# Optimization experiments

Hardware: AMD Instinct MI355X
Metric: run time of the kernel (lower is better)

## Reference

```python
import jax, jax.numpy as jnp
import numpy as np

NUM_USERS = 100000
NUM_PROTO = 16
EMBD_DIM = 128
BATCH = 8192
SEQ = 50
MOMENTUM = 0.9


def _l2norm(x, axis=-1, eps=1e-12):
    # matches torch F.normalize: x / max(||x||, eps)
    n = jnp.linalg.norm(x, axis=axis, keepdims=True)
    return x / jnp.maximum(n, eps)


def setup_inputs() -> dict:
    key = jax.random.key(0)
    k1, k2, k3, k4, k5 = jax.random.split(key, 5)
    user_idx = jnp.arange(BATCH, dtype=jnp.int64 if jax.config.jax_enable_x64 else jnp.int32)
    features = jax.random.normal(k1, (BATCH, SEQ, EMBD_DIM), dtype=jnp.float32)
    success_mask = jax.random.uniform(k2, (BATCH, SEQ), dtype=jnp.float32)
    user_prototypes = jax.random.normal(k3, (NUM_USERS, NUM_PROTO, EMBD_DIM), dtype=jnp.float32)
    shared_prototypes = jax.random.normal(k4, (1, NUM_PROTO, EMBD_DIM), dtype=jnp.float32)
    interaction_count = jax.random.uniform(k5, (NUM_USERS,), dtype=jnp.float32) * 500.0
    return {
        "user_idx": user_idx,
        "features": features,
        "success_mask": success_mask,
        "user_prototypes": user_prototypes,
        "shared_prototypes": shared_prototypes,
        "interaction_count": interaction_count,
    }


def reference(user_idx, features, success_mask, user_prototypes, shared_prototypes, interaction_count):
    # ---- get_prototypes: gather + curriculum blend ----
    cnt = interaction_count[user_idx]                          # [B]
    w = jax.nn.sigmoid(cnt / 100.0 - 3.0)[:, None, None]       # [B,1,1]
    user_p = user_prototypes[user_idx]                         # [B,P,D] gather
    combined = w * user_p + (1.0 - w) * shared_prototypes      # [B,P,D]

    # ---- update_prototypes: momentum blend + normalize + scatter ----
    m = jnp.clip(MOMENTUM + cnt / 1000.0, MOMENTUM, 0.99)[:, None, None]  # [B,1,1]
    sm = success_mask[..., None]                               # [B,S,1]
    masked = features * sm                                     # [B,S,D]
    denom = jnp.maximum(jnp.sum(sm, axis=1), 1e-6)             # [B,1]
    upd = jnp.sum(masked, axis=1) / denom                      # [B,D]
    upd = _l2norm(upd)                                         # [B,D]
    upd_b = jnp.broadcast_to(upd[:, None, :], (upd.shape[0], NUM_PROTO, upd.shape[1]))  # [B,P,D]

    new_rows = m * user_p + (1.0 - m) * upd_b                  # [B,P,D]
    new_user_prototypes = user_prototypes.at[user_idx].set(new_rows)  # scatter write-back

    shared_upd = _l2norm(jnp.mean(upd_b, axis=0))              # [P,D]
    new_shared = MOMENTUM * shared_prototypes + (1.0 - MOMENTUM) * shared_upd[None]  # [1,P,D]

    new_interaction_count = interaction_count.at[user_idx].add(1.0)
    return combined, new_rows, new_user_prototypes, new_shared, new_interaction_count
```

## Files before the change

kernel.cpp:

```cpp
#include <hip/hip_runtime.h>

#define BATCH   8192
#define SEQ     50
#define DIM     128
#define NPROTO  16
#define NUSERS  100000
#define ROWF4   (NPROTO * DIM / 4)
#define DF4     (DIM / 4)

typedef float vf4 __attribute__((ext_vector_type(4)));

__global__ void k_fill_inv(int* __restrict__ inv) {
    int i = blockIdx.x * blockDim.x + threadIdx.x;
    if (i < NUSERS) inv[i] = -1;
}

__global__ void k_prep(const int* __restrict__ idx, const float* __restrict__ icount,
                       int* __restrict__ inv, float2* __restrict__ wm) {
    int b = blockIdx.x * blockDim.x + threadIdx.x;
    if (b >= BATCH) return;
    int u = idx[b];
    inv[u] = b;
    float cnt = icount[u];
    float w = 1.0f / (1.0f + expf(3.0f - cnt * 0.01f));
    float m = fminf(fmaxf(0.9f + cnt * 0.001f, 0.9f), 0.99f);
    wm[b] = make_float2(w, m);
}

__global__ void k_upd(const float* __restrict__ feat, const float* __restrict__ mask,
                      float* __restrict__ upd) {
    int t = threadIdx.x;
    int bb = t >> 5;
    int l = t & 31;
    int b = blockIdx.x * 4 + bb;
    const vf4* f4p = (const vf4*)(feat + (size_t)b * SEQ * DIM);
    const float* mk = mask + (size_t)b * SEQ;
    vf4 acc = {0.f, 0.f, 0.f, 0.f};
    float msum = 0.f;
    #pragma unroll 5
    for (int s = 0; s < SEQ; ++s) {
        float m = mk[s];
        vf4 v = __builtin_nontemporal_load(&f4p[s * DF4 + l]);
        acc += v * m;
        msum += m;
    }
    float inv_d = 1.0f / fmaxf(msum, 1e-6f);
    acc *= inv_d;
    float sq = acc.x*acc.x + acc.y*acc.y + acc.z*acc.z + acc.w*acc.w;
    for (int off = 16; off >= 1; off >>= 1)
        sq += __shfl_xor(sq, off, 32);
    float inv = 1.0f / fmaxf(sqrtf(sq), 1e-12f);
    acc *= inv;
    ((vf4*)(upd + (size_t)b * DIM))[l] = acc;
}

__global__ void k_partial(const float* __restrict__ upd, float* __restrict__ part) {
    int d = threadIdx.x;
    int j = blockIdx.x;
    float acc = 0.f;
    for (int b = j; b < BATCH; b += 128)
        acc += upd[(size_t)b * DIM + d];
    part[j * DIM + d] = acc;
}

__global__ void k_shared(const float* __restrict__ part, const float* __restrict__ sharedP,
                         float* __restrict__ out4) {
    __shared__ float red[DIM];
    int d = threadIdx.x;
    float s = 0.f;
    for (int j = 0; j < 128; ++j) s += part[j * DIM + d];
    float mean = s * (1.0f / (float)BATCH);
    red[d] = mean * mean;
    __syncthreads();
    for (int off = 64; off >= 1; off >>= 1) {
        if (d < off) red[d] += red[d + off];
        __syncthreads();
    }
    float normed = mean / fmaxf(sqrtf(red[0]), 1e-12f);
    for (int p = 0; p < NPROTO; ++p)
        out4[p * DIM + d] = 0.9f * sharedP[p * DIM + d] + 0.1f * normed;
}

__global__ void __launch_bounds__(256) k_mega(
        const int* __restrict__ inv, const float2* __restrict__ wm,
        const vf4* __restrict__ userP, const vf4* __restrict__ sharedP,
        const vf4* __restrict__ upd,
        vf4* __restrict__ out1, vf4* __restrict__ out2, vf4* __restrict__ out3) {
    int u = blockIdx.x;
    int b = inv[u];
    size_t base = (size_t)u * ROWF4;
    if (b < 0) {
        #pragma unroll
        for (int k = 0; k < 2; ++k) {
            int i = threadIdx.x + k * 256;
            vf4 v = __builtin_nontemporal_load(&userP[base + i]);
            __builtin_nontemporal_store(v, &out3[base + i]);
        }
    } else {
        float2 c2 = wm[b];
        float w = c2.x, m = c2.y;
        float w1 = 1.0f - w, m1 = 1.0f - m;
        size_t ob = (size_t)b * ROWF4;
        const vf4* ub = upd + (size_t)b * DF4;
        #pragma unroll
        for (int k = 0; k < 2; ++k) {
            int i = threadIdx.x + k * 256;
            vf4 p  = __builtin_nontemporal_load(&userP[base + i]);
            vf4 sh = sharedP[i];
            vf4 ud = ub[i & (DF4 - 1)];
            vf4 c  = w * p + w1 * sh;
            vf4 nr = m * p + m1 * ud;
            __builtin_nontemporal_store(c,  &out1[ob + i]);
            __builtin_nontemporal_store(nr, &out2[ob + i]);
            __builtin_nontemporal_store(nr, &out3[base + i]);
        }
    }
}

__global__ void k_copy1(const float* __restrict__ src, float* __restrict__ dst, int n) {
    int i = blockIdx.x * blockDim.x + threadIdx.x;
    if (i < n) dst[i] = src[i];
}

__global__ void k_inc(const int* __restrict__ idx, float* __restrict__ out5) {
    int i = blockIdx.x * blockDim.x + threadIdx.x;
    if (i < BATCH) atomicAdd(&out5[idx[i]], 1.0f);
}

extern "C" void kernel_launch(void* const* d_in, const int* in_sizes, int n_in,
                              void* d_out, int out_size, void* d_ws, size_t ws_size,
                              hipStream_t stream) {
    const int*   user_idx = (const int*)d_in[0];
    const float* features = (const float*)d_in[1];
    const float* smask    = (const float*)d_in[2];
    const float* userP    = (const float*)d_in[3];
    const float* sharedP  = (const float*)d_in[4];
    const float* icount   = (const float*)d_in[5];

    float* out = (float*)d_out;
    const size_t n1 = (size_t)BATCH * NPROTO * DIM;
    const size_t n3 = (size_t)NUSERS * NPROTO * DIM;
    float* out_combined = out;
    float* out_newrows  = out + n1;
    float* out_newproto = out + 2 * n1;
    float* out_shared   = out + 2 * n1 + n3;
    float* out_count    = out_shared + (size_t)NPROTO * DIM;

    float*  ws_upd  = (float*)d_ws;
    float*  ws_part = ws_upd + (size_t)BATCH * DIM;
    int*    ws_inv  = (int*)(ws_part + 128 * DIM);
    float2* ws_wm   = (float2*)(ws_inv + NUSERS);

    k_fill_inv<<<(NUSERS + 255) / 256, 256, 0, stream>>>(ws_inv);
    k_prep<<<(BATCH + 255) / 256, 256, 0, stream>>>(user_idx, icount, ws_inv, ws_wm);
    k_upd<<<BATCH / 4, 128, 0, stream>>>(features, smask, ws_upd);
    k_partial<<<128, 128, 0, stream>>>(ws_upd, ws_part);
    k_shared<<<1, 128, 0, stream>>>(ws_part, sharedP, out_shared);
    k_mega<<<NUSERS, 256, 0, stream>>>(ws_inv, ws_wm, (const vf4*)userP,
                                       (const vf4*)sharedP, (const vf4*)ws_upd,
                                       (vf4*)out_combined, (vf4*)out_newrows,
                                       (vf4*)out_newproto);
    k_copy1<<<(NUSERS + 255) / 256, 256, 0, stream>>>(icount, out_count, NUSERS);
    k_inc<<<(BATCH + 255) / 256, 256, 0, stream>>>(user_idx, out_count);
}
```

Before: 355.9 us.

## Fuse update computation into batch-indexed mega kernel and merge count kernels

Folds the per-row masked mean and normalization into the main blend/scatter kernel, so each batch block computes its update vector in LDS and immediately writes combined, new_rows and the scattered prototype row. Non-batch users get a separate block range that only copies. The count copy and increment are merged into the init and prep kernels, and the w/m coefficients are now computed inline. This removes several launches and the workspace round-trip for the update vector, at the cost of two block barriers and only 8 waves' worth of sequence parallelism per batch block.

```diff
diff --git a/kernel.cpp b/kernel.cpp
--- a/kernel.cpp
+++ b/kernel.cpp
@@ -10,48 +10,103 @@
 
 typedef float vf4 __attribute__((ext_vector_type(4)));
 
-__global__ void k_fill_inv(int* __restrict__ inv) {
+__global__ void k_init(const float* __restrict__ icount, int* __restrict__ inv,
+                       float* __restrict__ out_count) {
     int i = blockIdx.x * blockDim.x + threadIdx.x;
-    if (i < NUSERS) inv[i] = -1;
+    if (i < NUSERS) {
+        inv[i] = -1;
+        out_count[i] = icount[i];
+    }
 }
 
-__global__ void k_prep(const int* __restrict__ idx, const float* __restrict__ icount,
-                       int* __restrict__ inv, float2* __restrict__ wm) {
+__global__ void k_prep(const int* __restrict__ idx, int* __restrict__ inv,
+                       float* __restrict__ out_count) {
     int b = blockIdx.x * blockDim.x + threadIdx.x;
     if (b >= BATCH) return;
     int u = idx[b];
     inv[u] = b;
-    float cnt = icount[u];
-    float w = 1.0f / (1.0f + expf(3.0f - cnt * 0.01f));
-    float m = fminf(fmaxf(0.9f + cnt * 0.001f, 0.9f), 0.99f);
-    wm[b] = make_float2(w, m);
+    atomicAdd(&out_count[u], 1.0f);
 }
 
-__global__ void k_upd(const float* __restrict__ feat, const float* __restrict__ mask,
-                      float* __restrict__ upd) {
+__global__ void __launch_bounds__(256) k_mega(
+        const int* __restrict__ idx, const int* __restrict__ inv,
+        const float* __restrict__ icount,
+        const float* __restrict__ feat, const float* __restrict__ mask,
+        const vf4* __restrict__ userP, const vf4* __restrict__ sharedP,
+        float* __restrict__ upd,
+        vf4* __restrict__ out1, vf4* __restrict__ out2, vf4* __restrict__ out3) {
+    int bid = blockIdx.x;
     int t = threadIdx.x;
-    int bb = t >> 5;
+
+    if (bid >= BATCH) {
+        int u = bid - BATCH;
+        if (inv[u] >= 0) return;
+        size_t base = (size_t)u * ROWF4;
+        #pragma unroll
+        for (int k = 0; k < 2; ++k) {
+            int i = t + k * 256;
+            vf4 v = __builtin_nontemporal_load(&userP[base + i]);
+            __builtin_nontemporal_store(v, &out3[base + i]);
+        }
+        return;
+    }
+
+    int b = bid;
+    int u = idx[b];
+
+    __shared__ vf4  lds_acc[8][32];
+    __shared__ float lds_m[8];
+    __shared__ vf4  lds_upd[32];
+
     int l = t & 31;
-    int b = blockIdx.x * 4 + bb;
+    int g = t >> 5;
     const vf4* f4p = (const vf4*)(feat + (size_t)b * SEQ * DIM);
     const float* mk = mask + (size_t)b * SEQ;
     vf4 acc = {0.f, 0.f, 0.f, 0.f};
     float msum = 0.f;
-    #pragma unroll 5
-    for (int s = 0; s < SEQ; ++s) {
+    for (int s = g; s < SEQ; s += 8) {
         float m = mk[s];
-        vf4 v = __builtin_nontemporal_load(&f4p[s * DF4 + l]);
-        acc += v * m;
+        acc += __builtin_nontemporal_load(&f4p[s * DF4 + l]) * m;
         msum += m;
     }
-    float inv_d = 1.0f / fmaxf(msum, 1e-6f);
-    acc *= inv_d;
-    float sq = acc.x*acc.x + acc.y*acc.y + acc.z*acc.z + acc.w*acc.w;
-    for (int off = 16; off >= 1; off >>= 1)
-        sq += __shfl_xor(sq, off, 32);
-    float inv = 1.0f / fmaxf(sqrtf(sq), 1e-12f);
-    acc *= inv;
-    ((vf4*)(upd + (size_t)b * DIM))[l] = acc;
+    lds_acc[g][l] = acc;
+    if (l == 0) lds_m[g] = msum;
+    __syncthreads();
+    if (t < 32) {
+        vf4 a = lds_acc[0][t];
+        #pragma unroll
+        for (int gg = 1; gg < 8; ++gg) a += lds_acc[gg][t];
+        float ms = lds_m[0];
+        #pragma unroll
+        for (int gg = 1; gg < 8; ++gg) ms += lds_m[gg];
+        a *= 1.0f / fmaxf(ms, 1e-6f);
+        float sq = a.x*a.x + a.y*a.y + a.z*a.z + a.w*a.w;
+        for (int off = 16; off >= 1; off >>= 1)
+            sq += __shfl_xor(sq, off, 32);
+        a *= 1.0f / fmaxf(sqrtf(sq), 1e-12f);
+        lds_upd[t] = a;
+        ((vf4*)(upd + (size_t)b * DIM))[t] = a;
+    }
+    __syncthreads();
+
+    float cnt = icount[u];
+    float w = 1.0f / (1.0f + expf(3.0f - cnt * 0.01f));
+    float m = fminf(fmaxf(0.9f + cnt * 0.001f, 0.9f), 0.99f);
+    float w1 = 1.0f - w, m1 = 1.0f - m;
+    size_t base = (size_t)u * ROWF4;
+    size_t ob   = (size_t)b * ROWF4;
+    #pragma unroll
+    for (int k = 0; k < 2; ++k) {
+        int i = t + k * 256;
+        vf4 p  = __builtin_nontemporal_load(&userP[base + i]);
+        vf4 sh = sharedP[i];
+        vf4 ud = lds_upd[i & (DF4 - 1)];
+        vf4 c  = w * p + w1 * sh;
+        vf4 nr = m * p + m1 * ud;
+        __builtin_nontemporal_store(c,  &out1[ob + i]);
+        __builtin_nontemporal_store(nr, &out2[ob + i]);
+        __builtin_nontemporal_store(nr, &out3[base + i]);
+    }
 }
 
 __global__ void k_partial(const float* __restrict__ upd, float* __restrict__ part) {
@@ -81,52 +136,6 @@
         out4[p * DIM + d] = 0.9f * sharedP[p * DIM + d] + 0.1f * normed;
 }
 
-__global__ void __launch_bounds__(256) k_mega(
-        const int* __restrict__ inv, const float2* __restrict__ wm,
-        const vf4* __restrict__ userP, const vf4* __restrict__ sharedP,
-        const vf4* __restrict__ upd,
-        vf4* __restrict__ out1, vf4* __restrict__ out2, vf4* __restrict__ out3) {
-    int u = blockIdx.x;
-    int b = inv[u];
-    size_t base = (size_t)u * ROWF4;
-    if (b < 0) {
-        #pragma unroll
-        for (int k = 0; k < 2; ++k) {
-            int i = threadIdx.x + k * 256;
-            vf4 v = __builtin_nontemporal_load(&userP[base + i]);
-            __builtin_nontemporal_store(v, &out3[base + i]);
-        }
-    } else {
-        float2 c2 = wm[b];
-        float w = c2.x, m = c2.y;
-        float w1 = 1.0f - w, m1 = 1.0f - m;
-        size_t ob = (size_t)b * ROWF4;
-        const vf4* ub = upd + (size_t)b * DF4;
-        #pragma unroll
-        for (int k = 0; k < 2; ++k) {
-            int i = threadIdx.x + k * 256;
-            vf4 p  = __builtin_nontemporal_load(&userP[base + i]);
-            vf4 sh = sharedP[i];
-            vf4 ud = ub[i & (DF4 - 1)];
-            vf4 c  = w * p + w1 * sh;
-            vf4 nr = m * p + m1 * ud;
-            __builtin_nontemporal_store(c,  &out1[ob + i]);
-            __builtin_nontemporal_store(nr, &out2[ob + i]);
-            __builtin_nontemporal_store(nr, &out3[base + i]);
-        }
-    }
-}
-
-__global__ void k_copy1(const float* __restrict__ src, float* __restrict__ dst, int n) {
-    int i = blockIdx.x * blockDim.x + threadIdx.x;
-    if (i < n) dst[i] = src[i];
-}
-
-__global__ void k_inc(const int* __restrict__ idx, float* __restrict__ out5) {
-    int i = blockIdx.x * blockDim.x + threadIdx.x;
-    if (i < BATCH) atomicAdd(&out5[idx[i]], 1.0f);
-}
-
 extern "C" void kernel_launch(void* const* d_in, const int* in_sizes, int n_in,
                               void* d_out, int out_size, void* d_ws, size_t ws_size,
                               hipStream_t stream) {
@@ -146,20 +155,18 @@
     float* out_shared   = out + 2 * n1 + n3;
     float* out_count    = out_shared + (size_t)NPROTO * DIM;
 
-    float*  ws_upd  = (float*)d_ws;
-    float*  ws_part = ws_upd + (size_t)BATCH * DIM;
-    int*    ws_inv  = (int*)(ws_part + 128 * DIM);
-    float2* ws_wm   = (float2*)(ws_inv + NUSERS);
+    float* ws_upd  = (float*)d_ws;
+    float* ws_part = ws_upd + (size_t)BATCH * DIM;
+    int*   ws_inv  = (int*)(ws_part + 128 * DIM);
 
-    k_fill_inv<<<(NUSERS + 255) / 256, 256, 0, stream>>>(ws_inv);
-    k_prep<<<(BATCH + 255) / 256, 256, 0, stream>>>(user_idx, icount, ws_inv, ws_wm);
-    k_upd<<<BATCH / 4, 128, 0, stream>>>(features, smask, ws_upd);
+    k_init<<<(NUSERS + 255) / 256, 256, 0, stream>>>(icount, ws_inv, out_count);
+    k_prep<<<(BATCH + 255) / 256, 256, 0, stream>>>(user_idx, ws_inv, out_count);
+    k_mega<<<BATCH + NUSERS, 256, 0, stream>>>(user_idx, ws_inv, icount,
+                                               features, smask,
+                                               (const vf4*)userP, (const vf4*)sharedP,
+                                               ws_upd,
+                                               (vf4*)out_combined, (vf4*)out_newrows,
+                                               (vf4*)out_newproto);
     k_partial<<<128, 128, 0, stream>>>(ws_upd, ws_part);
     k_shared<<<1, 128, 0, stream>>>(ws_part, sharedP, out_shared);
-    k_mega<<<NUSERS, 256, 0, stream>>>(ws_inv, ws_wm, (const vf4*)userP,
-                                       (const vf4*)sharedP, (const vf4*)ws_upd,
-                                       (vf4*)out_combined, (vf4*)out_newrows,
-                                       (vf4*)out_newproto);
-    k_copy1<<<(NUSERS + 255) / 256, 256, 0, stream>>>(icount, out_count, NUSERS);
-    k_inc<<<(BATCH + 255) / 256, 256, 0, stream>>>(user_idx, out_count);
 }
```

New measurement: 356.1 us. About the same (+0.1%).
